# Kernel tuning notes

Hardware: AMD Instinct MI355X
Metric: run time of the kernel (lower is better)

## Reference

```python
import jax, jax.numpy as jnp
import numpy as np

B, H, S, D = 2, 16, 2048, 64
N_SINK = 1


def setup_inputs() -> dict:
    key = jax.random.key(0)
    kq, kk, ks = jax.random.split(key, 3)
    q = jax.random.normal(kq, (B, H, S, D), dtype=jnp.float32)
    k = jax.random.normal(kk, (B, H, S, D), dtype=jnp.float32)
    sinks = jax.random.normal(ks, (B, H, S, N_SINK), dtype=jnp.float32)
    return {"q": q, "k": k, "sinks": sinks}


def reference(q, k, sinks):
    # scores: [B,H,S,S] = q @ k^T
    scores = jnp.einsum("bhqd,bhkd->bhqk", q, k)
    # per-key norm ||k||, broadcast over query dim: [B,H,1,S]
    denom = jnp.sqrt(jnp.sum(k * k, axis=-1))[..., None, :]
    w = scores / denom
    # causal: zero (NOT -inf) above the diagonal, faithful to torch.tril
    w = jnp.tril(w)
    # append learned sink logits: [B,H,S,S+N_SINK]
    w = jnp.concatenate([w, sinks], axis=-1)
    return jax.nn.softmax(w, axis=-1)
```

## Files before the change

### kernel.cpp

```cpp
#include <hip/hip_runtime.h>
#include <hip/hip_fp16.h>
#include <math.h>

#define S 2048
#define D 64
#define BH 32
#define TILE 64
#define NT (S / TILE)
#define SP1 (S + 1)

typedef _Float16 f16;
typedef f16 f16x8 __attribute__((ext_vector_type(8)));
typedef f16 f16x4 __attribute__((ext_vector_type(4)));
typedef float f32x4 __attribute__((ext_vector_type(4)));

#define LDS_PITCH 72

__global__ __launch_bounds__(256) void knorm_kernel(const float* __restrict__ k,
                                                    float* __restrict__ rinv) {
    int row  = (blockIdx.x * 256 + threadIdx.x) >> 6;
    int lane = threadIdx.x & 63;
    float v = k[(size_t)row * D + lane];
    float s = v * v;
    #pragma unroll
    for (int off = 32; off; off >>= 1) s += __shfl_xor(s, off);
    if (lane == 0) rinv[row] = 1.0f / sqrtf(s);
}

__global__ __launch_bounds__(256) void rowsum_kernel(
    const float* __restrict__ q, const float* __restrict__ k,
    const float* __restrict__ sinks, const float* __restrict__ rinv,
    float* __restrict__ inv_l)
{
    __shared__ __align__(16) f16 qs[TILE * LDS_PITCH];
    __shared__ __align__(16) f16 ks[TILE * LDS_PITCH];

    const int it = blockIdx.x;
    const int bh = blockIdx.y;
    const int i0 = it * TILE;
    const int tid  = threadIdx.x;
    const int lane = tid & 63;
    const int w    = tid >> 6;
    const int m    = lane & 15;
    const int quad = lane >> 4;

    const float* qbase = q + (size_t)bh * S * D;
    const float* kbase = k + (size_t)bh * S * D;

    {
        int r  = tid >> 4;
        int c4 = (tid & 15) * 4;
        #pragma unroll
        for (int rb = 0; rb < 4; rb++) {
            int row = rb * 16 + r;
            float4 v = *(const float4*)(qbase + (size_t)(i0 + row) * D + c4);
            f16x4 hv; hv[0] = (f16)v.x; hv[1] = (f16)v.y; hv[2] = (f16)v.z; hv[3] = (f16)v.w;
            *(f16x4*)&qs[row * LDS_PITCH + c4] = hv;
        }
    }
    __syncthreads();

    f16x8 a0 = *(const f16x8*)&qs[(w * 16 + m) * LDS_PITCH + 0  + quad * 8];
    f16x8 a1 = *(const f16x8*)&qs[(w * 16 + m) * LDS_PITCH + 32 + quad * 8];

    float rowsum[4] = {0.f, 0.f, 0.f, 0.f};
    const int ib = i0 + w * 16 + quad * 4;

    for (int jt = 0; jt <= it; jt++) {
        const int j0 = jt * TILE;
        __syncthreads();
        {
            int r  = tid >> 4;
            int c4 = (tid & 15) * 4;
            #pragma unroll
            for (int rb = 0; rb < 4; rb++) {
                int row = rb * 16 + r;
                float4 v = *(const float4*)(kbase + (size_t)(j0 + row) * D + c4);
                f16x4 hv; hv[0] = (f16)v.x; hv[1] = (f16)v.y; hv[2] = (f16)v.z; hv[3] = (f16)v.w;
                *(f16x4*)&ks[row * LDS_PITCH + c4] = hv;
            }
        }
        __syncthreads();

        const bool diag = (jt == it);
        #pragma unroll
        for (int st = 0; st < 4; st++) {
            f16x8 b0 = *(const f16x8*)&ks[(st * 16 + m) * LDS_PITCH + 0  + quad * 8];
            f16x8 b1 = *(const f16x8*)&ks[(st * 16 + m) * LDS_PITCH + 32 + quad * 8];
            f32x4 acc = {0.f, 0.f, 0.f, 0.f};
            acc = __builtin_amdgcn_mfma_f32_16x16x32_f16(a0, b0, acc, 0, 0, 0);
            acc = __builtin_amdgcn_mfma_f32_16x16x32_f16(a1, b1, acc, 0, 0, 0);
            const int j = j0 + st * 16 + m;
            const float rj = rinv[bh * S + j];
            #pragma unroll
            for (int r = 0; r < 4; r++) {
                float e = __expf(acc[r] * rj);
                if (diag && j > ib + r) e = 0.0f;
                rowsum[r] += e;
            }
        }
    }

    #pragma unroll
    for (int off = 1; off < 16; off <<= 1)
        #pragma unroll
        for (int r = 0; r < 4; r++) rowsum[r] += __shfl_xor(rowsum[r], off);

    if (m == 0) {
        #pragma unroll
        for (int r = 0; r < 4; r++) {
            int i = ib + r;
            float l = rowsum[r] + (float)(S - 1 - i) + __expf(sinks[bh * S + i]);
            inv_l[bh * S + i] = 1.0f / l;
        }
    }
}

__global__ __launch_bounds__(256) void out_kernel(
    const float* __restrict__ q, const float* __restrict__ k,
    const float* __restrict__ rinv, const float* __restrict__ inv_l,
    float* __restrict__ out)
{
    const int jt = blockIdx.x;
    const int it = blockIdx.y;
    const int bh = blockIdx.z;
    const int i0 = it * TILE, j0 = jt * TILE;
    const int tid = threadIdx.x;
    float* obase = out + (size_t)bh * S * SP1;

    if (jt > it) {
        const int rb = tid >> 6;
        const int c  = tid & 63;
        #pragma unroll
        for (int r = 0; r < 16; r++) {
            int i = i0 + rb * 16 + r;
            obase[(size_t)i * SP1 + j0 + c] = inv_l[bh * S + i];
        }
        return;
    }

    __shared__ __align__(16) f16 qs[TILE * LDS_PITCH];
    __shared__ __align__(16) f16 ks[TILE * LDS_PITCH];

    const int lane = tid & 63;
    const int w    = tid >> 6;
    const int m    = lane & 15;
    const int quad = lane >> 4;

    const float* qbase = q + (size_t)bh * S * D;
    const float* kbase = k + (size_t)bh * S * D;

    {
        int r  = tid >> 4;
        int c4 = (tid & 15) * 4;
        #pragma unroll
        for (int rb = 0; rb < 4; rb++) {
            int row = rb * 16 + r;
            float4 vq = *(const float4*)(qbase + (size_t)(i0 + row) * D + c4);
            f16x4 hq; hq[0] = (f16)vq.x; hq[1] = (f16)vq.y; hq[2] = (f16)vq.z; hq[3] = (f16)vq.w;
            *(f16x4*)&qs[row * LDS_PITCH + c4] = hq;
            float4 vk = *(const float4*)(kbase + (size_t)(j0 + row) * D + c4);
            f16x4 hk; hk[0] = (f16)vk.x; hk[1] = (f16)vk.y; hk[2] = (f16)vk.z; hk[3] = (f16)vk.w;
            *(f16x4*)&ks[row * LDS_PITCH + c4] = hk;
        }
    }
    __syncthreads();

    f16x8 a0 = *(const f16x8*)&qs[(w * 16 + m) * LDS_PITCH + 0  + quad * 8];
    f16x8 a1 = *(const f16x8*)&qs[(w * 16 + m) * LDS_PITCH + 32 + quad * 8];

    const int ib = i0 + w * 16 + quad * 4;
    float il[4];
    #pragma unroll
    for (int r = 0; r < 4; r++) il[r] = inv_l[bh * S + ib + r];

    const bool diag = (jt == it);
    #pragma unroll
    for (int st = 0; st < 4; st++) {
        f16x8 b0 = *(const f16x8*)&ks[(st * 16 + m) * LDS_PITCH + 0  + quad * 8];
        f16x8 b1 = *(const f16x8*)&ks[(st * 16 + m) * LDS_PITCH + 32 + quad * 8];
        f32x4 acc = {0.f, 0.f, 0.f, 0.f};
        acc = __builtin_amdgcn_mfma_f32_16x16x32_f16(a0, b0, acc, 0, 0, 0);
        acc = __builtin_amdgcn_mfma_f32_16x16x32_f16(a1, b1, acc, 0, 0, 0);
        const int j = j0 + st * 16 + m;
        const float rj = rinv[bh * S + j];
        #pragma unroll
        for (int r = 0; r < 4; r++) {
            float val = __expf(acc[r] * rj) * il[r];
            if (diag && j > ib + r) val = il[r];
            obase[(size_t)(ib + r) * SP1 + j] = val;
        }
    }
}

__global__ __launch_bounds__(256) void sink_kernel(const float* __restrict__ sinks,
                                                   const float* __restrict__ inv_l,
                                                   float* __restrict__ out) {
    int t = blockIdx.x * 256 + threadIdx.x;
    out[(size_t)t * SP1 + S] = __expf(sinks[t]) * inv_l[t];
}

extern "C" void kernel_launch(void* const* d_in, const int* in_sizes, int n_in,
                              void* d_out, int out_size, void* d_ws, size_t ws_size,
                              hipStream_t stream) {
    const float* q     = (const float*)d_in[0];
    const float* k     = (const float*)d_in[1];
    const float* sinks = (const float*)d_in[2];
    float* out = (float*)d_out;

    float* rinv  = (float*)d_ws;
    float* inv_l = rinv + BH * S;

    knorm_kernel<<<dim3(BH * S / 4), 256, 0, stream>>>(k, rinv);
    rowsum_kernel<<<dim3(NT, BH), 256, 0, stream>>>(q, k, sinks, rinv, inv_l);
    out_kernel<<<dim3(NT, NT, BH), 256, 0, stream>>>(q, k, rinv, inv_l, out);
    sink_kernel<<<dim3(BH * S / 256), 256, 0, stream>>>(sinks, inv_l, out);
}
```

Before: 786.1 us.

## Fuse row-sum, output and sink kernels into one per-row-tile kernel

Merges the row-sum pass, the tiled output pass and the sink-column kernel into a single kernel. Each block owns a 64-row query tile, first computes the softmax denominators and keeps them in shared memory, then recomputes the score tiles and writes the full output row-tile, including the constant above-diagonal region and the sink column. Blocks are launched in reverse row-tile order so the heavy late tiles start first. This removes two launches and the global inv_l round trip. In exchange, the store-heavy output phase now runs on only 1024 blocks instead of a much larger grid, which may reduce memory-level parallelism.

```diff
diff --git a/kernel.cpp b/kernel.cpp
--- a/kernel.cpp
+++ b/kernel.cpp
@@ -27,15 +27,16 @@
     if (lane == 0) rinv[row] = 1.0f / sqrtf(s);
 }
 
-__global__ __launch_bounds__(256) void rowsum_kernel(
+__global__ __launch_bounds__(256) void fused_kernel(
     const float* __restrict__ q, const float* __restrict__ k,
     const float* __restrict__ sinks, const float* __restrict__ rinv,
-    float* __restrict__ inv_l)
+    float* __restrict__ out)
 {
     __shared__ __align__(16) f16 qs[TILE * LDS_PITCH];
     __shared__ __align__(16) f16 ks[TILE * LDS_PITCH];
+    __shared__ float ils[TILE];
 
-    const int it = blockIdx.x;
+    const int it = NT - 1 - blockIdx.x;
     const int bh = blockIdx.y;
     const int i0 = it * TILE;
     const int tid  = threadIdx.x;
@@ -46,6 +47,8 @@
 
     const float* qbase = q + (size_t)bh * S * D;
     const float* kbase = k + (size_t)bh * S * D;
+    const float* rbase = rinv + (size_t)bh * S;
+    float* obase = out + (size_t)bh * S * SP1;
 
     {
         int r  = tid >> 4;
@@ -63,9 +66,9 @@
     f16x8 a0 = *(const f16x8*)&qs[(w * 16 + m) * LDS_PITCH + 0  + quad * 8];
     f16x8 a1 = *(const f16x8*)&qs[(w * 16 + m) * LDS_PITCH + 32 + quad * 8];
 
-    float rowsum[4] = {0.f, 0.f, 0.f, 0.f};
     const int ib = i0 + w * 16 + quad * 4;
 
+    float rowsum[4] = {0.f, 0.f, 0.f, 0.f};
     for (int jt = 0; jt <= it; jt++) {
         const int j0 = jt * TILE;
         __syncthreads();
@@ -91,7 +94,7 @@
             acc = __builtin_amdgcn_mfma_f32_16x16x32_f16(a0, b0, acc, 0, 0, 0);
             acc = __builtin_amdgcn_mfma_f32_16x16x32_f16(a1, b1, acc, 0, 0, 0);
             const int j = j0 + st * 16 + m;
-            const float rj = rinv[bh * S + j];
+            const float rj = rbase[j];
             #pragma unroll
             for (int r = 0; r < 4; r++) {
                 float e = __expf(acc[r] * rj);
@@ -111,93 +114,63 @@
         for (int r = 0; r < 4; r++) {
             int i = ib + r;
             float l = rowsum[r] + (float)(S - 1 - i) + __expf(sinks[bh * S + i]);
-            inv_l[bh * S + i] = 1.0f / l;
-        }
-    }
-}
-
-__global__ __launch_bounds__(256) void out_kernel(
-    const float* __restrict__ q, const float* __restrict__ k,
-    const float* __restrict__ rinv, const float* __restrict__ inv_l,
-    float* __restrict__ out)
-{
-    const int jt = blockIdx.x;
-    const int it = blockIdx.y;
-    const int bh = blockIdx.z;
-    const int i0 = it * TILE, j0 = jt * TILE;
-    const int tid = threadIdx.x;
-    float* obase = out + (size_t)bh * S * SP1;
-
-    if (jt > it) {
-        const int rb = tid >> 6;
-        const int c  = tid & 63;
-        #pragma unroll
-        for (int r = 0; r < 16; r++) {
-            int i = i0 + rb * 16 + r;
-            obase[(size_t)i * SP1 + j0 + c] = inv_l[bh * S + i];
-        }
-        return;
-    }
-
-    __shared__ __align__(16) f16 qs[TILE * LDS_PITCH];
-    __shared__ __align__(16) f16 ks[TILE * LDS_PITCH];
-
-    const int lane = tid & 63;
-    const int w    = tid >> 6;
-    const int m    = lane & 15;
-    const int quad = lane >> 4;
-
-    const float* qbase = q + (size_t)bh * S * D;
-    const float* kbase = k + (size_t)bh * S * D;
-
-    {
-        int r  = tid >> 4;
-        int c4 = (tid & 15) * 4;
-        #pragma unroll
-        for (int rb = 0; rb < 4; rb++) {
-            int row = rb * 16 + r;
-            float4 vq = *(const float4*)(qbase + (size_t)(i0 + row) * D + c4);
-            f16x4 hq; hq[0] = (f16)vq.x; hq[1] = (f16)vq.y; hq[2] = (f16)vq.z; hq[3] = (f16)vq.w;
-            *(f16x4*)&qs[row * LDS_PITCH + c4] = hq;
-            float4 vk = *(const float4*)(kbase + (size_t)(j0 + row) * D + c4);
-            f16x4 hk; hk[0] = (f16)vk.x; hk[1] = (f16)vk.y; hk[2] = (f16)vk.z; hk[3] = (f16)vk.w;
-            *(f16x4*)&ks[row * LDS_PITCH + c4] = hk;
+            ils[w * 16 + quad * 4 + r] = 1.0f / l;
         }
     }
     __syncthreads();
 
-    f16x8 a0 = *(const f16x8*)&qs[(w * 16 + m) * LDS_PITCH + 0  + quad * 8];
-    f16x8 a1 = *(const f16x8*)&qs[(w * 16 + m) * LDS_PITCH + 32 + quad * 8];
+    if (tid < TILE) {
+        int i = i0 + tid;
+        obase[(size_t)i * SP1 + S] = __expf(sinks[bh * S + i]) * ils[tid];
+    }
 
-    const int ib = i0 + w * 16 + quad * 4;
     float il[4];
     #pragma unroll
-    for (int r = 0; r < 4; r++) il[r] = inv_l[bh * S + ib + r];
+    for (int r = 0; r < 4; r++) il[r] = ils[w * 16 + quad * 4 + r];
 
-    const bool diag = (jt == it);
-    #pragma unroll
-    for (int st = 0; st < 4; st++) {
-        f16x8 b0 = *(const f16x8*)&ks[(st * 16 + m) * LDS_PITCH + 0  + quad * 8];
-        f16x8 b1 = *(const f16x8*)&ks[(st * 16 + m) * LDS_PITCH + 32 + quad * 8];
-        f32x4 acc = {0.f, 0.f, 0.f, 0.f};
-        acc = __builtin_amdgcn_mfma_f32_16x16x32_f16(a0, b0, acc, 0, 0, 0);
-        acc = __builtin_amdgcn_mfma_f32_16x16x32_f16(a1, b1, acc, 0, 0, 0);
-        const int j = j0 + st * 16 + m;
-        const float rj = rinv[bh * S + j];
-        #pragma unroll
-        for (int r = 0; r < 4; r++) {
-            float val = __expf(acc[r] * rj) * il[r];
-            if (diag && j > ib + r) val = il[r];
-            obase[(size_t)(ib + r) * SP1 + j] = val;
+    for (int jt = 0; jt < NT; jt++) {
+        const int j0 = jt * TILE;
+        if (jt <= it) {
+            __syncthreads();
+            {
+                int r  = tid >> 4;
+                int c4 = (tid & 15) * 4;
+                #pragma unroll
+                for (int rb = 0; rb < 4; rb++) {
+                    int row = rb * 16 + r;
+                    float4 v = *(const float4*)(kbase + (size_t)(j0 + row) * D + c4);
+                    f16x4 hv; hv[0] = (f16)v.x; hv[1] = (f16)v.y; hv[2] = (f16)v.z; hv[3] = (f16)v.w;
+                    *(f16x4*)&ks[row * LDS_PITCH + c4] = hv;
+                }
+            }
+            __syncthreads();
+
+            const bool diag = (jt == it);
+            #pragma unroll
+            for (int st = 0; st < 4; st++) {
+                f16x8 b0 = *(const f16x8*)&ks[(st * 16 + m) * LDS_PITCH + 0  + quad * 8];
+                f16x8 b1 = *(const f16x8*)&ks[(st * 16 + m) * LDS_PITCH + 32 + quad * 8];
+                f32x4 acc = {0.f, 0.f, 0.f, 0.f};
+                acc = __builtin_amdgcn_mfma_f32_16x16x32_f16(a0, b0, acc, 0, 0, 0);
+                acc = __builtin_amdgcn_mfma_f32_16x16x32_f16(a1, b1, acc, 0, 0, 0);
+                const int j = j0 + st * 16 + m;
+                const float rj = rbase[j];
+                #pragma unroll
+                for (int r = 0; r < 4; r++) {
+                    float val = __expf(acc[r] * rj) * il[r];
+                    if (diag && j > ib + r) val = il[r];
+                    obase[(size_t)(ib + r) * SP1 + j] = val;
+                }
+            }
+        } else {
+            const int cb = lane;
+            #pragma unroll
+            for (int r = 0; r < 16; r++) {
+                int row = w * 16 + r;
+                obase[(size_t)(i0 + row) * SP1 + j0 + cb] = ils[row];
+            }
         }
     }
-}
-
-__global__ __launch_bounds__(256) void sink_kernel(const float* __restrict__ sinks,
-                                                   const float* __restrict__ inv_l,
-                                                   float* __restrict__ out) {
-    int t = blockIdx.x * 256 + threadIdx.x;
-    out[(size_t)t * SP1 + S] = __expf(sinks[t]) * inv_l[t];
 }
 
 extern "C" void kernel_launch(void* const* d_in, const int* in_sizes, int n_in,
@@ -208,11 +181,8 @@
     const float* sinks = (const float*)d_in[2];
     float* out = (float*)d_out;
 
-    float* rinv  = (float*)d_ws;
-    float* inv_l = rinv + BH * S;
+    float* rinv = (float*)d_ws;
 
     knorm_kernel<<<dim3(BH * S / 4), 256, 0, stream>>>(k, rinv);
-    rowsum_kernel<<<dim3(NT, BH), 256, 0, stream>>>(q, k, sinks, rinv, inv_l);
-    out_kernel<<<dim3(NT, NT, BH), 256, 0, stream>>>(q, k, rinv, inv_l, out);
-    sink_kernel<<<dim3(BH * S / 256), 256, 0, stream>>>(sinks, inv_l, out);
+    fused_kernel<<<dim3(NT, BH), 256, 0, stream>>>(q, k, sinks, rinv, out);
 }
```

After: 723.9 us. 7.9% less time.
